# Performance work log

Hardware: AMD Instinct MI355X
Metric: run time of the kernel (lower is better)

The kernel has to match this reference:

```python
import jax, jax.numpy as jnp
import numpy as np

B, C = 2, 2
D = H = W = 192
N_BIF = 64                 # bif ids 0..63; labels = bif*4 + stub (stub in 1..3)
NUM_LABELS = 4 * N_BIF     # 256
MIN_STUBS = 2
MIN_VOXELS = 1
TEMP = 0.2


def setup_inputs() -> dict:
    key = jax.random.key(0)
    k1, k2 = jax.random.split(key)
    pred = jax.random.normal(k1, (B, C, D, H, W), dtype=jnp.float32)
    stub_label_map = jax.random.randint(k2, (B, 1, D, H, W), 0, NUM_LABELS).astype(jnp.float32)
    return {"pred": pred, "stub_label_map": stub_label_map}


def reference(pred, stub_label_map):
    # foreground probability: softmax over channel dim, take class 1
    fg = jax.nn.softmax(pred, axis=1)[:, 1]                     # [B,D,H,W]
    labels = jnp.round(stub_label_map[:, 0]).astype(jnp.int32)  # [B,D,H,W]

    Bn = fg.shape[0]
    fg_flat = fg.reshape(Bn, -1)
    lab_flat = labels.reshape(Bn, -1)

    seg = lambda v, i: jax.ops.segment_sum(v, i, num_segments=NUM_LABELS)
    sums = jax.vmap(seg)(fg_flat, lab_flat)                      # [B, NUM_LABELS]
    counts = jax.vmap(seg)(jnp.ones_like(fg_flat), lab_flat)     # [B, NUM_LABELS]

    # group labels as [bif, stub]; drop bif 0 and stub 0 (never used in loop)
    sums = sums.reshape(Bn, N_BIF, 4)[:, 1:, 1:4]                # [B, N_BIF-1, 3]
    counts = counts.reshape(Bn, N_BIF, 4)[:, 1:, 1:4]

    valid = counts >= MIN_VOXELS                                 # stub has enough voxels
    means = sums / jnp.maximum(counts, 1.0)                      # per-stub mean fg prob

    # softmin over the valid stubs of each bif (masked softmax of -mean/temp)
    logits = jnp.where(valid, -means / TEMP, -1e9)
    weights = jax.nn.softmax(logits, axis=-1)
    score = jnp.sum(jnp.where(valid, means * weights, 0.0), axis=-1)  # [B, N_BIF-1]

    valid_bif = jnp.sum(valid, axis=-1) >= MIN_STUBS
    total = jnp.sum(jnp.where(valid_bif, 1.0 - score, 0.0))
    n_bifs = jnp.sum(valid_bif)
    return jnp.where(n_bifs > 0, total / jnp.maximum(n_bifs, 1).astype(total.dtype), 0.0)
```

## Files before the change

kernel.cpp:

```cpp
#include <hip/hip_runtime.h>
#include <math.h>

#define BATCH     2
#define NLAB      256
#define VOX       (192*192*192)
#define VVEC      (VOX/4)
#define TEMP      0.2f
#define GRIDX     256
#define NITER     (VVEC/(GRIDX*256))
#define NPART     16

#define STEP      4096.0f
#define INV_STEP  (1.0f/4096.0f)

__global__ __launch_bounds__(256) void histo_kernel(
    const float* __restrict__ pred,
    const float* __restrict__ labmap,
    float* __restrict__ ws_slots)
{
    __shared__ float s_hist[2 * NLAB];

    const int b = blockIdx.y;
    const int tid = threadIdx.x;

    s_hist[tid] = 0.0f;
    s_hist[tid + NLAB] = 0.0f;
    __syncthreads();

    const float4* p0 = (const float4*)(pred + (size_t)b * 2 * VOX);
    const float4* p1 = (const float4*)(pred + (size_t)b * 2 * VOX + VOX);
    const float4* lm = (const float4*)(labmap + (size_t)b * VOX);

    const int copy = (tid & 1) << 8;
    const int base = blockIdx.x * 256 + tid;

    #pragma unroll 3
    for (int it = 0; it < NITER; ++it) {
        const int i = base + it * (GRIDX * 256);
        float4 a = p0[i];
        float4 c = p1[i];
        float4 l = lm[i];

        float fg0 = 1.0f / (1.0f + __expf(a.x - c.x));
        float fg1 = 1.0f / (1.0f + __expf(a.y - c.y));
        float fg2 = 1.0f / (1.0f + __expf(a.z - c.z));
        float fg3 = 1.0f / (1.0f + __expf(a.w - c.w));

        int l0 = ((int)(l.x + 0.5f)) & (NLAB - 1);
        int l1 = ((int)(l.y + 0.5f)) & (NLAB - 1);
        int l2 = ((int)(l.z + 0.5f)) & (NLAB - 1);
        int l3 = ((int)(l.w + 0.5f)) & (NLAB - 1);

        if ((l0 & 3) && l0 >= 4) atomicAdd(&s_hist[copy + l0], STEP + fg0);
        if ((l1 & 3) && l1 >= 4) atomicAdd(&s_hist[copy + l1], STEP + fg1);
        if ((l2 & 3) && l2 >= 4) atomicAdd(&s_hist[copy + l2], STEP + fg2);
        if ((l3 & 3) && l3 >= 4) atomicAdd(&s_hist[copy + l3], STEP + fg3);
    }
    __syncthreads();

    ws_slots[((size_t)(b * GRIDX + blockIdx.x)) * NLAB + tid] =
        s_hist[tid] + s_hist[tid + NLAB];
}

__global__ __launch_bounds__(256) void reduce_kernel(
    const float* __restrict__ ws_slots,
    float* __restrict__ psum,
    float* __restrict__ pcnt)
{
    const int bin  = threadIdx.x;
    const int b    = blockIdx.x / NPART;
    const int part = blockIdx.x % NPART;
    const int per  = GRIDX / NPART;

    float cs = 0.0f, ss = 0.0f;
    for (int s = part * per; s < (part + 1) * per; ++s) {
        float v = ws_slots[((size_t)(b * GRIDX + s)) * NLAB + bin];
        float c = floorf(v * INV_STEP + 0.5f);
        cs += c;
        ss += v - c * STEP;
    }
    psum[(size_t)blockIdx.x * NLAB + bin] = ss;
    pcnt[(size_t)blockIdx.x * NLAB + bin] = cs;
}

__global__ __launch_bounds__(256) void scalar_kernel(
    const float* __restrict__ psum,
    const float* __restrict__ pcnt,
    float* __restrict__ out)
{
    __shared__ float s_fsum[BATCH][NLAB];
    __shared__ float s_fcnt[BATCH][NLAB];

    const int tid = threadIdx.x;

    for (int b = 0; b < BATCH; ++b) {
        float ss = 0.0f, cs = 0.0f;
        for (int p = 0; p < NPART; ++p) {
            ss += psum[(size_t)(b * NPART + p) * NLAB + tid];
            cs += pcnt[(size_t)(b * NPART + p) * NLAB + tid];
        }
        s_fsum[b][tid] = ss;
        s_fcnt[b][tid] = cs;
    }
    __syncthreads();

    if (tid < 64) {
        float total = 0.0f;
        float nbifs = 0.0f;
        if (tid >= 1) {
            for (int bb = 0; bb < BATCH; ++bb) {
                float means[3];
                bool  valid[3];
                int   nvalid = 0;
                for (int s = 0; s < 3; ++s) {
                    int lab = tid * 4 + 1 + s;
                    float cnt = s_fcnt[bb][lab];
                    float sum = s_fsum[bb][lab];
                    valid[s] = (cnt >= 1.0f);
                    means[s] = sum / fmaxf(cnt, 1.0f);
                    nvalid  += valid[s] ? 1 : 0;
                }
                float logits[3], m = -3e38f;
                for (int s = 0; s < 3; ++s) {
                    logits[s] = valid[s] ? (-means[s] / TEMP) : -1e9f;
                    m = fmaxf(m, logits[s]);
                }
                float e[3], se = 0.0f;
                for (int s = 0; s < 3; ++s) { e[s] = __expf(logits[s] - m); se += e[s]; }
                float score = 0.0f;
                for (int s = 0; s < 3; ++s) {
                    if (valid[s]) score += means[s] * (e[s] / se);
                }
                if (nvalid >= 2) {
                    total += 1.0f - score;
                    nbifs += 1.0f;
                }
            }
        }
        for (int off = 32; off > 0; off >>= 1) {
            total += __shfl_down(total, off);
            nbifs += __shfl_down(nbifs, off);
        }
        if (tid == 0) {
            out[0] = (nbifs > 0.0f) ? (total / fmaxf(nbifs, 1.0f)) : 0.0f;
        }
    }
}

extern "C" void kernel_launch(void* const* d_in, const int* in_sizes, int n_in,
                              void* d_out, int out_size, void* d_ws, size_t ws_size,
                              hipStream_t stream) {
    const float* pred = (const float*)d_in[0];
    const float* lab  = (const float*)d_in[1];

    float* ws_slots = (float*)d_ws;
    float* psum = ws_slots + (size_t)BATCH * GRIDX * NLAB;
    float* pcnt = psum + (size_t)BATCH * NPART * NLAB;

    dim3 grid(GRIDX, BATCH);
    histo_kernel<<<grid, 256, 0, stream>>>(pred, lab, ws_slots);
    reduce_kernel<<<BATCH * NPART, 256, 0, stream>>>(ws_slots, psum, pcnt);
    scalar_kernel<<<1, 256, 0, stream>>>(psum, pcnt, (float*)d_out);
}
```

Baseline: 206.1 us.

## Replace LDS atomic histogram with MFMA one-hot matrix-multiply accumulation

Each voxel's foreground probability (rounded to bf16) and its label are packed into one 32-bit word and staged per wave in shared memory. The histogram is then built with bf16 MFMA: one-hot high/low label-nibble matrices are multiplied to accumulate counts and probability sums in registers, which replaces the contended shared-memory float atomics. The grid grows from 256 to 768 blocks with an occupancy hint. In exchange, the fg probabilities lose precision through bf16, and label 0 and stub 0 are no longer filtered in the hot loop.

```diff
diff --git a/kernel.cpp b/kernel.cpp
--- a/kernel.cpp
+++ b/kernel.cpp
@@ -4,62 +4,110 @@
 #define BATCH     2
 #define NLAB      256
 #define VOX       (192*192*192)
-#define VVEC      (VOX/4)
 #define TEMP      0.2f
-#define GRIDX     256
-#define NITER     (VVEC/(GRIDX*256))
+#define GRIDX     768
+#define NITER     (VOX / (GRIDX * 1024))
 #define NPART     16
 
 #define STEP      4096.0f
 #define INV_STEP  (1.0f/4096.0f)
 
-__global__ __launch_bounds__(256) void histo_kernel(
+typedef unsigned int u32;
+typedef __attribute__((ext_vector_type(8))) short bf16x8;
+typedef __attribute__((ext_vector_type(4))) float f32x4;
+union FragU { uint4 u; bf16x8 v; };
+
+__device__ __forceinline__ u32 packvox(float pa, float pc, float pl) {
+    const float fg = 1.0f / (1.0f + __expf(pa - pc));
+    u32 bits = __float_as_uint(fg);
+    bits += 0x7FFFu + ((bits >> 16) & 1u);
+    const u32 lab = ((u32)(int)(pl + 0.5f)) & 255u;
+    return (lab << 24) | (bits >> 16);
+}
+
+#define PAIR(de, dodd, aw, b1w, b2w) do {                                   \
+    const u32 _e = (de), _o = (dodd);                                       \
+    const bool he  = ((_e >> 28) == mlane);                                 \
+    const bool ho  = ((_o >> 28) == mlane);                                 \
+    const bool le  = (((_e >> 24) & 15u) == mlane);                         \
+    const bool lo_ = (((_o >> 24) & 15u) == mlane);                         \
+    aw  = (he ? 0x00003F80u : 0u) | (ho  ? 0x3F800000u : 0u);               \
+    b1w = (le ? 0x00003F80u : 0u) | (lo_ ? 0x3F800000u : 0u);               \
+    b2w = (le ? (_e & 0xFFFFu) : 0u) | (lo_ ? (_o << 16) : 0u);             \
+} while (0)
+
+__global__ __launch_bounds__(256, 4) void histo_kernel(
     const float* __restrict__ pred,
     const float* __restrict__ labmap,
     float* __restrict__ ws_slots)
 {
-    __shared__ float s_hist[2 * NLAB];
-
-    const int b = blockIdx.y;
-    const int tid = threadIdx.x;
-
-    s_hist[tid] = 0.0f;
-    s_hist[tid + NLAB] = 0.0f;
-    __syncthreads();
+    __shared__ __align__(16) u32 s_stage[4][2][256];
+    __shared__ float s_cnt[4][NLAB];
+    __shared__ float s_sum[4][NLAB];
+
+    const int b    = blockIdx.y;
+    const int tid  = threadIdx.x;
+    const int w    = tid >> 6;
+    const int lane = tid & 63;
+    const u32 mlane = (u32)(lane & 15);
+    const int g    = lane >> 4;
 
     const float4* p0 = (const float4*)(pred + (size_t)b * 2 * VOX);
     const float4* p1 = (const float4*)(pred + (size_t)b * 2 * VOX + VOX);
     const float4* lm = (const float4*)(labmap + (size_t)b * VOX);
 
-    const int copy = (tid & 1) << 8;
+    f32x4 accC = {0.f, 0.f, 0.f, 0.f};
+    f32x4 accS = {0.f, 0.f, 0.f, 0.f};
+
     const int base = blockIdx.x * 256 + tid;
 
-    #pragma unroll 3
+    #pragma unroll 2
     for (int it = 0; it < NITER; ++it) {
         const int i = base + it * (GRIDX * 256);
-        float4 a = p0[i];
-        float4 c = p1[i];
-        float4 l = lm[i];
-
-        float fg0 = 1.0f / (1.0f + __expf(a.x - c.x));
-        float fg1 = 1.0f / (1.0f + __expf(a.y - c.y));
-        float fg2 = 1.0f / (1.0f + __expf(a.z - c.z));
-        float fg3 = 1.0f / (1.0f + __expf(a.w - c.w));
-
-        int l0 = ((int)(l.x + 0.5f)) & (NLAB - 1);
-        int l1 = ((int)(l.y + 0.5f)) & (NLAB - 1);
-        int l2 = ((int)(l.z + 0.5f)) & (NLAB - 1);
-        int l3 = ((int)(l.w + 0.5f)) & (NLAB - 1);
-
-        if ((l0 & 3) && l0 >= 4) atomicAdd(&s_hist[copy + l0], STEP + fg0);
-        if ((l1 & 3) && l1 >= 4) atomicAdd(&s_hist[copy + l1], STEP + fg1);
-        if ((l2 & 3) && l2 >= 4) atomicAdd(&s_hist[copy + l2], STEP + fg2);
-        if ((l3 & 3) && l3 >= 4) atomicAdd(&s_hist[copy + l3], STEP + fg3);
+        const float4 a = p0[i];
+        const float4 c = p1[i];
+        const float4 l = lm[i];
+
+        uint4 pkv;
+        pkv.x = packvox(a.x, c.x, l.x);
+        pkv.y = packvox(a.y, c.y, l.y);
+        pkv.z = packvox(a.z, c.z, l.z);
+        pkv.w = packvox(a.w, c.w, l.w);
+
+        u32* st = &s_stage[w][it & 1][0];
+        *(uint4*)(st + (lane << 2)) = pkv;
+
+        const u32* rp = st + (g << 3);
+        #pragma unroll
+        for (int t = 0; t < 8; ++t) {
+            const uint4 q0 = *(const uint4*)(rp + t * 32);
+            const uint4 q1 = *(const uint4*)(rp + t * 32 + 4);
+            u32 a0, a1, a2, a3, b10, b11, b12, b13, b20, b21, b22, b23;
+            PAIR(q0.x, q0.y, a0, b10, b20);
+            PAIR(q0.z, q0.w, a1, b11, b21);
+            PAIR(q1.x, q1.y, a2, b12, b22);
+            PAIR(q1.z, q1.w, a3, b13, b23);
+            FragU A, B1, B2;
+            A.u  = make_uint4(a0, a1, a2, a3);
+            B1.u = make_uint4(b10, b11, b12, b13);
+            B2.u = make_uint4(b20, b21, b22, b23);
+            accC = __builtin_amdgcn_mfma_f32_16x16x32_bf16(A.v, B1.v, accC, 0, 0, 0);
+            accS = __builtin_amdgcn_mfma_f32_16x16x32_bf16(A.v, B2.v, accS, 0, 0, 0);
+        }
+    }
+
+    const int row0 = (lane >> 4) << 2;
+    const int colb = lane & 15;
+    #pragma unroll
+    for (int j = 0; j < 4; ++j) {
+        s_cnt[w][(row0 + j) * 16 + colb] = accC[j];
+        s_sum[w][(row0 + j) * 16 + colb] = accS[j];
     }
     __syncthreads();
 
-    ws_slots[((size_t)(b * GRIDX + blockIdx.x)) * NLAB + tid] =
-        s_hist[tid] + s_hist[tid + NLAB];
+    const float cs = s_cnt[0][tid] + s_cnt[1][tid] + s_cnt[2][tid] + s_cnt[3][tid];
+    const float ss = s_sum[0][tid] + s_sum[1][tid] + s_sum[2][tid] + s_sum[3][tid];
+    ws_slots[((size_t)(b * GRIDX + blockIdx.x)) * NLAB + tid] = ss + STEP * cs;
 }
 
 __global__ __launch_bounds__(256) void reduce_kernel(
```

Result: slower. 217.1 us (+5.3%).
